# Performance work log

Hardware: AMD Instinct MI355X
Metric: run time of the kernel (lower is better)

Reference implementation:

```python
import jax, jax.numpy as jnp
import numpy as np

NB = 5  # number of graph nodes per image
COUNT_THRESH = 10000  # min pixel count for a region to be selected
BOX_DOWNSCALE = 16.0  # backbone stride


def _masks_to_boxes(mask_np, ids):
    # torchvision.ops.masks_to_boxes: (xmin, ymin, xmax, ymax) in pixel coords
    boxes = []
    for oid in ids:
        ys, xs = np.nonzero(mask_np == oid)
        boxes.append([xs.min(), ys.min(), xs.max(), ys.max()])
    return np.asarray(boxes, dtype=np.float32)


def _select_boxes(seg_logits):
    # mask = espnet(x).max(1)[1]; original code only keeps boxes from the LAST
    # batch element (loop variable overwritten each iteration) -- preserved here.
    mask = np.asarray(jnp.argmax(seg_logits, axis=1))[-1]
    ids, counts = np.unique(mask, return_counts=True)
    ids, counts = ids[1:], counts[1:]  # drop background / first label
    boxes = _masks_to_boxes(mask, ids) / BOX_DOWNSCALE  # feature-map coords
    # rr = argsort(argsort(counts, descending)) == rank of each region by size
    rr = np.argsort(np.argsort(-counts))
    sel = []
    for idx in range(len(boxes)):
        for b_idx in range(len(rr)):
            if idx == rr[b_idx] and counts[b_idx] > COUNT_THRESH and len(sel) < NB - 2:
                sel.append(b_idx)
                break
    return boxes.astype(np.int64), sel


def setup_inputs() -> dict:
    key = jax.random.key(0)
    k1, k2, k3 = jax.random.split(key, 3)
    N, K, Hin, Win = 4, 20, 480, 640   # even H/W -> parity padding is a no-op
    C, H, W = 512, Hin // 16, Win // 16  # stride-16 VGG backbone features
    return {
        "seg_logits": jax.random.normal(k1, (N, K, Hin, Win), jnp.float32),
        "feat": jax.random.normal(k2, (N, C, H, W), jnp.float32),
        "pool_x": jax.random.normal(k3, (N, C), jnp.float32),
    }


def reference(seg_logits, feat, pool_x):
    boxes, sel = _select_boxes(seg_logits)
    N, C, H, W = feat.shape
    # Selected-region crops; boxes identical for every batch element (original
    # bug), so each crop+resize is vectorized over the batch dim.
    nodes = []
    for b in sel:
        x0, y0, x1, y1 = [int(v) for v in boxes[b]]
        crop = feat[:, :, y0:y1, x0:x1]
        nodes.append(jax.image.resize(crop, (N, C, H, W), "bilinear"))
    # Fixed fallback boxes (center, left/top/right/bottom strips)
    bb = [[W // 4, H // 4, 3 * W // 4, 3 * H // 4],
          [0, 0, W // 3, H],
          [0, 0, W, H // 3],
          [2 * W // 3, 0, W, H],
          [0, 2 * H // 3, W, H]]
    if len(nodes) < NB:
        for i in range(len(bb) - len(nodes)):  # range evaluated once, as in original
            x0, y0, x1, y1 = bb[i]
            crop = feat[:, :, y0:y1, x0:x1]
            nodes.append(jax.image.resize(crop, (N, C, H, W), "bilinear"))
    graph_nodes = jnp.stack(nodes, axis=1)  # [N, NB, C, H, W]
    # Original: graph_nodes.view(NB, N, ...) is a raw reshape, then cat with feat
    x_cropped = jnp.concatenate(
        [graph_nodes.reshape(NB, N, C, H, W), feat[None]], axis=0)  # [NB+1,N,C,H,W]
    return pool_x, NB, N, x_cropped
```

## Files before the change

### kernel.cpp

```cpp
#include <hip/hip_runtime.h>
#include <hip/hip_bf16.h>

#define K_CLS 20
#define HIN 480
#define WIN 640
#define NPIX (HIN * WIN)
#define C_ 512
#define H_ 30
#define W_ 40
#define HW_ (H_ * W_)
#define NB_ 5
#define CNT_THRESH 10000
#define XCROP_ELEMS (6 * 4 * C_ * H_ * W_)
#define ELEMS_PER_SN (C_ * H_ * W_)
#define OUT_TOTAL (2050 + XCROP_ELEMS)

#define NBLK_STATS 300
#define NODE_OFF (NBLK_STATS * 100)

typedef float f32x2 __attribute__((ext_vector_type(2)));
typedef float f32x4 __attribute__((ext_vector_type(4)));

#define OUT_CPB 4
#define OUT_CGRP (C_ / OUT_CPB)
#define OUT_TPB 256
#define OUT_BLOCKS (24 * OUT_CGRP)


__global__ void stats_k(const float* __restrict__ seg, int* __restrict__ ws) {
    __shared__ int s_cnt[K_CLS], s_mnx[K_CLS], s_mny[K_CLS], s_mxx[K_CLS], s_mxy[K_CLS];
    int t = threadIdx.x;
    if (t < K_CLS) { s_cnt[t] = 0; s_mnx[t] = WIN; s_mny[t] = HIN; s_mxx[t] = -1; s_mxy[t] = -1; }
    __syncthreads();

    int p = blockIdx.x * blockDim.x + t;
    const float4* base = (const float4*)(seg + (size_t)3 * K_CLS * NPIX) + p;
    float4 v = base[0];
    float b0 = v.x, b1 = v.y, b2 = v.z, b3 = v.w;
    int k0 = 0, k1 = 0, k2 = 0, k3 = 0;
    #pragma unroll
    for (int k = 1; k < K_CLS; k++) {
        float4 u = base[(size_t)k * (NPIX / 4)];
        if (u.x > b0) { b0 = u.x; k0 = k; }
        if (u.y > b1) { b1 = u.y; k1 = k; }
        if (u.z > b2) { b2 = u.z; k2 = k; }
        if (u.w > b3) { b3 = u.w; k3 = k; }
    }
    int x = (p * 4) % WIN, y = (p * 4) / WIN;
    if (k0 == k1 && k1 == k2 && k2 == k3) {
        atomicAdd(&s_cnt[k0], 4);
        atomicMin(&s_mnx[k0], x);     atomicMax(&s_mxx[k0], x + 3);
        atomicMin(&s_mny[k0], y);     atomicMax(&s_mxy[k0], y);
    } else {
        int ks[4] = {k0, k1, k2, k3};
        #pragma unroll
        for (int i = 0; i < 4; i++) {
            atomicAdd(&s_cnt[ks[i]], 1);
            atomicMin(&s_mnx[ks[i]], x + i);  atomicMax(&s_mxx[ks[i]], x + i);
            atomicMin(&s_mny[ks[i]], y);      atomicMax(&s_mxy[ks[i]], y);
        }
    }
    __syncthreads();
    if (t < 100) {
        int a = t / 20, c = t % 20;
        int val = (a == 0) ? s_cnt[c] : (a == 1) ? s_mnx[c] : (a == 2) ? s_mny[c]
                : (a == 3) ? s_mxx[c] : s_mxy[c];
        ws[blockIdx.x * 100 + t] = val;
    }
}

__global__ void plan_k(int* __restrict__ ws, const float* __restrict__ pool_x,
                       float* __restrict__ out) {
    __shared__ int part[10][100];
    __shared__ int st[100];
    int t = threadIdx.x;

    ((float2*)out)[t] = ((const float2*)pool_x)[t];
    if (t == 0) { out[2048] = 5.0f; out[2049] = 4.0f; }

    if (t < 1000) {
        int c = t % 100, chunk = t / 100;
        int a = c / 20;
        int acc = (a == 0) ? 0 : (a == 1) ? WIN : (a == 2) ? HIN : -1;
        #pragma unroll
        for (int i = 0; i < 30; i++) {
            int v = ws[(chunk * 30 + i) * 100 + c];
            if (a == 0)      acc += v;
            else if (a <= 2) acc = v < acc ? v : acc;
            else             acc = v > acc ? v : acc;
        }
        part[chunk][c] = acc;
    }
    __syncthreads();
    if (t < 100) {
        int a = t / 20;
        int acc = part[0][t];
        #pragma unroll
        for (int i = 1; i < 10; i++) {
            int v = part[i][t];
            if (a == 0)      acc += v;
            else if (a <= 2) acc = v < acc ? v : acc;
            else             acc = v > acc ? v : acc;
        }
        st[t] = acc;
    }
    __syncthreads();
    if (t != 0) return;

    int* cnt = st;
    int* mnx = st + 20; int* mny = st + 40; int* mxx = st + 60; int* mxy = st + 80;
    int* nb  = ws + NODE_OFF;

    int firstp = -1;
    for (int i = 0; i < K_CLS; i++) if (cnt[i] > 0) { firstp = i; break; }
    int order[K_CLS]; int nc = 0;
    for (int i = 0; i < K_CLS; i++)
        if (cnt[i] > 0 && i != firstp) order[nc++] = i;

    for (int i = 1; i < nc; i++) {
        int key = order[i]; int j = i - 1;
        while (j >= 0 && cnt[order[j]] < cnt[key]) { order[j + 1] = order[j]; j--; }
        order[j + 1] = key;
    }

    int nsel = 0;
    for (int i = 0; i < nc && nsel < NB_ - 2; i++) {
        int b = order[i];
        if (cnt[b] > CNT_THRESH) {
            nb[nsel * 4 + 0] = mnx[b] >> 4;
            nb[nsel * 4 + 1] = mny[b] >> 4;
            nb[nsel * 4 + 2] = mxx[b] >> 4;
            nb[nsel * 4 + 3] = mxy[b] >> 4;
            nsel++;
        }
    }
    const int bb[5][4] = {
        {W_ / 4, H_ / 4, 3 * W_ / 4, 3 * H_ / 4},
        {0, 0, W_ / 3, H_},
        {0, 0, W_, H_ / 3},
        {2 * W_ / 3, 0, W_, H_},
        {0, 2 * H_ / 3, W_, H_}
    };
    for (int i = 0; nsel < NB_; i++, nsel++) {
        nb[nsel * 4 + 0] = bb[i][0];
        nb[nsel * 4 + 1] = bb[i][1];
        nb[nsel * 4 + 2] = bb[i][2];
        nb[nsel * 4 + 3] = bb[i][3];
    }
}

__global__ __launch_bounds__(OUT_TPB) void out_k(const float* __restrict__ feat,
                      const int* __restrict__ nb,
                      float* __restrict__ out) {
    __shared__ float sf[OUT_CPB * HW_];
    int sn = blockIdx.x / OUT_CGRP;
    int c0 = (blockIdx.x % OUT_CGRP) * OUT_CPB;
    float* obase = out + 2050 + (size_t)sn * ELEMS_PER_SN + (size_t)c0 * HW_;

    if (sn >= 20) {
        const float* src = feat + ((size_t)(sn - 20) * C_ + c0) * HW_;
        for (int i = threadIdx.x; i < (OUT_CPB * HW_) / 2; i += OUT_TPB) {
            __builtin_nontemporal_store(((const f32x2*)src)[i], (f32x2*)obase + i);
        }
        return;
    }

    int b  = sn % NB_;
    int n  = sn / NB_;
    int x0 = nb[b * 4 + 0], y0 = nb[b * 4 + 1];
    int x1 = nb[b * 4 + 2], y1 = nb[b * 4 + 3];
    int iw = x1 - x0; if (iw < 1) iw = 1;
    int ih = y1 - y0; if (ih < 1) ih = 1;

    const float* src = feat + ((size_t)n * C_ + c0) * HW_;
    for (int i = threadIdx.x; i < (OUT_CPB * HW_) / 4; i += OUT_TPB) {
        ((f32x4*)sf)[i] = ((const f32x4*)src)[i];
    }
    __syncthreads();

    float sx = (float)iw * (1.0f / (float)W_);
    float sy = (float)ih * (1.0f / (float)H_);
    int cb = y0 * W_ + x0;

    for (int hw = threadIdx.x; hw < HW_; hw += OUT_TPB) {
        int h = hw / W_;
        int w = hw - h * W_;

        float fy  = ((float)h + 0.5f) * sy - 0.5f;
        float flY = floorf(fy);
        float ty  = fy - flY;
        int ylo_u = (int)flY;
        int ylo = max(ylo_u, 0);
        int yhi = min(ylo_u + 1, ih - 1);

        float fx  = ((float)w + 0.5f) * sx - 0.5f;
        float flX = floorf(fx);
        float tx  = fx - flX;
        int xlo_u = (int)flX;
        int xlo = max(xlo_u, 0);
        int xhi = min(xlo_u + 1, iw - 1);

        int i00 = cb + ylo * W_ + xlo, i01 = cb + ylo * W_ + xhi;
        int i10 = cb + yhi * W_ + xlo, i11 = cb + yhi * W_ + xhi;

        float* op = obase + hw;
        #pragma unroll
        for (int j = 0; j < OUT_CPB; j++) {
            const float* sp = sf + j * HW_;
            float v00 = sp[i00], v01 = sp[i01];
            float v10 = sp[i10], v11 = sp[i11];
            float top = v00 + tx * (v01 - v00);
            float bot = v10 + tx * (v11 - v10);
            __builtin_nontemporal_store(top + ty * (bot - top), op + j * HW_);
        }
    }
}

extern "C" void kernel_launch(void* const* d_in, const int* in_sizes, int n_in,
                              void* d_out, int out_size, void* d_ws, size_t ws_size,
                              hipStream_t stream) {
    const float* seg    = (const float*)d_in[0];
    const float* feat   = (const float*)d_in[1];
    const float* pool_x = (const float*)d_in[2];
    float* out = (float*)d_out;
    int* ws = (int*)d_ws;

    stats_k<<<NBLK_STATS, 256, 0, stream>>>(seg, ws);
    plan_k<<<1, 1024, 0, stream>>>(ws, pool_x, out);
    out_k<<<OUT_BLOCKS, OUT_TPB, 0, stream>>>(feat, ws + NODE_OFF, out);
}
```

Before: 196.9 us.

## Fuse per-node crop-resize and feat copy into one block per channel group

```diff
diff --git a/kernel.cpp b/kernel.cpp
--- a/kernel.cpp
+++ b/kernel.cpp
@@ -21,10 +21,10 @@
 typedef float f32x2 __attribute__((ext_vector_type(2)));
 typedef float f32x4 __attribute__((ext_vector_type(4)));
 
-#define OUT_CPB 4
-#define OUT_CGRP (C_ / OUT_CPB)
-#define OUT_TPB 256
-#define OUT_BLOCKS (24 * OUT_CGRP)
+#define F_CPB 4
+#define F_CGRP (C_ / F_CPB)
+#define F_TPB 512
+#define F_BLOCKS (4 * F_CGRP)
 
 
 __global__ void stats_k(const float* __restrict__ seg, int* __restrict__ ws) {
@@ -149,69 +149,86 @@
     }
 }
 
-__global__ __launch_bounds__(OUT_TPB) void out_k(const float* __restrict__ feat,
+__global__ __launch_bounds__(F_TPB) void fuse_k(const float* __restrict__ feat,
                       const int* __restrict__ nb,
                       float* __restrict__ out) {
-    __shared__ float sf[OUT_CPB * HW_];
-    int sn = blockIdx.x / OUT_CGRP;
-    int c0 = (blockIdx.x % OUT_CGRP) * OUT_CPB;
-    float* obase = out + 2050 + (size_t)sn * ELEMS_PER_SN + (size_t)c0 * HW_;
-
-    if (sn >= 20) {
-        const float* src = feat + ((size_t)(sn - 20) * C_ + c0) * HW_;
-        for (int i = threadIdx.x; i < (OUT_CPB * HW_) / 2; i += OUT_TPB) {
-            __builtin_nontemporal_store(((const f32x2*)src)[i], (f32x2*)obase + i);
-        }
-        return;
-    }
-
-    int b  = sn % NB_;
-    int n  = sn / NB_;
-    int x0 = nb[b * 4 + 0], y0 = nb[b * 4 + 1];
-    int x1 = nb[b * 4 + 2], y1 = nb[b * 4 + 3];
-    int iw = x1 - x0; if (iw < 1) iw = 1;
-    int ih = y1 - y0; if (ih < 1) ih = 1;
+    __shared__ float sf[F_CPB * HW_];
+    __shared__ int   s_xlo[NB_ * W_], s_xhi[NB_ * W_];
+    __shared__ float s_tx [NB_ * W_];
+    __shared__ int   s_r0 [NB_ * H_], s_r1 [NB_ * H_];
+    __shared__ float s_ty [NB_ * H_];
+
+    int t  = threadIdx.x;
+    int n  = blockIdx.x / F_CGRP;
+    int c0 = (blockIdx.x % F_CGRP) * F_CPB;
 
     const float* src = feat + ((size_t)n * C_ + c0) * HW_;
-    for (int i = threadIdx.x; i < (OUT_CPB * HW_) / 4; i += OUT_TPB) {
-        ((f32x4*)sf)[i] = ((const f32x4*)src)[i];
-    }
-    __syncthreads();
-
-    float sx = (float)iw * (1.0f / (float)W_);
-    float sy = (float)ih * (1.0f / (float)H_);
-    int cb = y0 * W_ + x0;
-
-    for (int hw = threadIdx.x; hw < HW_; hw += OUT_TPB) {
-        int h = hw / W_;
-        int w = hw - h * W_;
-
-        float fy  = ((float)h + 0.5f) * sy - 0.5f;
-        float flY = floorf(fy);
-        float ty  = fy - flY;
-        int ylo_u = (int)flY;
-        int ylo = max(ylo_u, 0);
-        int yhi = min(ylo_u + 1, ih - 1);
-
-        float fx  = ((float)w + 0.5f) * sx - 0.5f;
-        float flX = floorf(fx);
-        float tx  = fx - flX;
-        int xlo_u = (int)flX;
-        int xlo = max(xlo_u, 0);
-        int xhi = min(xlo_u + 1, iw - 1);
-
-        int i00 = cb + ylo * W_ + xlo, i01 = cb + ylo * W_ + xhi;
-        int i10 = cb + yhi * W_ + xlo, i11 = cb + yhi * W_ + xhi;
-
-        float* op = obase + hw;
-        #pragma unroll
-        for (int j = 0; j < OUT_CPB; j++) {
-            const float* sp = sf + j * HW_;
-            float v00 = sp[i00], v01 = sp[i01];
-            float v10 = sp[i10], v11 = sp[i11];
-            float top = v00 + tx * (v01 - v00);
-            float bot = v10 + tx * (v11 - v10);
-            __builtin_nontemporal_store(top + ty * (bot - top), op + j * HW_);
+    float* cdst = out + 2050 + (size_t)(20 + n) * ELEMS_PER_SN + (size_t)c0 * HW_;
+    for (int i = t; i < (F_CPB * HW_) / 4; i += F_TPB) {
+        f32x4 v = ((const f32x4*)src)[i];
+        ((f32x4*)sf)[i] = v;
+        f32x2 lo = {v.x, v.y}, hi = {v.z, v.w};
+        __builtin_nontemporal_store(lo, (f32x2*)(cdst + i * 4));
+        __builtin_nontemporal_store(hi, (f32x2*)(cdst + i * 4 + 2));
+    }
+
+    if (t < NB_ * W_ + NB_ * H_) {
+        int isX = t < NB_ * W_;
+        int b   = isX ? t / W_ : (t - NB_ * W_) / H_;
+        int x0 = nb[b * 4 + 0], y0 = nb[b * 4 + 1];
+        int x1 = nb[b * 4 + 2], y1 = nb[b * 4 + 3];
+        int iw = max(x1 - x0, 1), ih = max(y1 - y0, 1);
+        if (isX) {
+            int w = t % W_;
+            float fx = ((float)w + 0.5f) * (float)iw / (float)W_ - 0.5f;
+            float fl = floorf(fx);
+            int lo_u = (int)fl;
+            s_tx[t]  = fx - fl;
+            s_xlo[t] = max(lo_u, 0);
+            s_xhi[t] = min(lo_u + 1, iw - 1);
+        } else {
+            int e = t - NB_ * W_;
+            int h = e % H_;
+            float fy = ((float)h + 0.5f) * (float)ih / (float)H_ - 0.5f;
+            float fl = floorf(fy);
+            int lo_u = (int)fl;
+            int yl = max(lo_u, 0);
+            int yh = min(lo_u + 1, ih - 1);
+            int cb = y0 * W_ + x0;
+            s_ty[e] = fy - fl;
+            s_r0[e] = cb + yl * W_;
+            s_r1[e] = cb + yh * W_;
+        }
+    }
+    __syncthreads();
+
+    for (int b = 0; b < NB_; b++) {
+        float* ob = out + 2050 + (size_t)(5 * n + b) * ELEMS_PER_SN + (size_t)c0 * HW_;
+        const int*   xlo = s_xlo + b * W_;
+        const int*   xhi = s_xhi + b * W_;
+        const float* txp = s_tx  + b * W_;
+        const int*   r0p = s_r0  + b * H_;
+        const int*   r1p = s_r1  + b * H_;
+        const float* typ = s_ty  + b * H_;
+        for (int hw = t; hw < HW_; hw += F_TPB) {
+            int h = hw / W_;
+            int w = hw - h * W_;
+            int r0 = r0p[h], r1 = r1p[h];
+            float ty = typ[h];
+            int xl = xlo[w], xh = xhi[w];
+            float tx = txp[w];
+            int i00 = r0 + xl, i01 = r0 + xh;
+            int i10 = r1 + xl, i11 = r1 + xh;
+            float* op = ob + hw;
+            #pragma unroll
+            for (int j = 0; j < F_CPB; j++) {
+                const float* sp = sf + j * HW_;
+                float v00 = sp[i00], v01 = sp[i01];
+                float v10 = sp[i10], v11 = sp[i11];
+                float top = v00 + tx * (v01 - v00);
+                float bot = v10 + tx * (v11 - v10);
+                __builtin_nontemporal_store(top + ty * (bot - top), op + j * HW_);
+            }
         }
     }
 }
@@ -227,5 +244,5 @@
 
     stats_k<<<NBLK_STATS, 256, 0, stream>>>(seg, ws);
     plan_k<<<1, 1024, 0, stream>>>(ws, pool_x, out);
-    out_k<<<OUT_BLOCKS, OUT_TPB, 0, stream>>>(feat, ws + NODE_OFF, out);
-}
+    fuse_k<<<F_BLOCKS, F_TPB, 0, stream>>>(feat, ws + NODE_OFF, out);
+}
```

Measured after the change: 199.6 us. No clear change (+1.4%).

## Fuse plan and output kernels, recomputing box plan redundantly per block

Applied to the files above, without the earlier changes.

```diff
diff --git a/kernel.cpp b/kernel.cpp
--- a/kernel.cpp
+++ b/kernel.cpp
@@ -16,15 +16,14 @@
 #define OUT_TOTAL (2050 + XCROP_ELEMS)
 
 #define NBLK_STATS 300
-#define NODE_OFF (NBLK_STATS * 100)
 
 typedef float f32x2 __attribute__((ext_vector_type(2)));
 typedef float f32x4 __attribute__((ext_vector_type(4)));
 
-#define OUT_CPB 4
-#define OUT_CGRP (C_ / OUT_CPB)
-#define OUT_TPB 256
-#define OUT_BLOCKS (24 * OUT_CGRP)
+#define F_CPB 4
+#define F_CGRP (C_ / F_CPB)
+#define F_TPB 512
+#define F_BLOCKS (4 * F_CGRP)
 
 
 __global__ void stats_k(const float* __restrict__ seg, int* __restrict__ ws) {
@@ -69,22 +68,41 @@
     }
 }
 
-__global__ void plan_k(int* __restrict__ ws, const float* __restrict__ pool_x,
-                       float* __restrict__ out) {
-    __shared__ int part[10][100];
+__global__ __launch_bounds__(F_TPB) void fuse_k(const float* __restrict__ feat,
+                      const int* __restrict__ ws,
+                      const float* __restrict__ pool_x,
+                      float* __restrict__ out) {
+    __shared__ float sf[F_CPB * HW_];
+    __shared__ int part[5][100];
     __shared__ int st[100];
-    int t = threadIdx.x;
-
-    ((float2*)out)[t] = ((const float2*)pool_x)[t];
-    if (t == 0) { out[2048] = 5.0f; out[2049] = 4.0f; }
-
-    if (t < 1000) {
+    __shared__ int s_nb[NB_ * 4];
+
+    int t  = threadIdx.x;
+    int n  = blockIdx.x / F_CGRP;
+    int c0 = (blockIdx.x % F_CGRP) * F_CPB;
+
+    const float* src = feat + ((size_t)n * C_ + c0) * HW_;
+    float* cdst = out + 2050 + (size_t)(20 + n) * ELEMS_PER_SN + (size_t)c0 * HW_;
+    for (int i = t; i < (F_CPB * HW_) / 4; i += F_TPB) {
+        f32x4 v = ((const f32x4*)src)[i];
+        ((f32x4*)sf)[i] = v;
+        f32x2 lo = {v.x, v.y}, hi = {v.z, v.w};
+        __builtin_nontemporal_store(lo, (f32x2*)(cdst + i * 4));
+        __builtin_nontemporal_store(hi, (f32x2*)(cdst + i * 4 + 2));
+    }
+    if (blockIdx.x == 0) {
+        for (int i = t; i < 1024; i += F_TPB)
+            ((float2*)out)[i] = ((const float2*)pool_x)[i];
+        if (t == 0) { out[2048] = 5.0f; out[2049] = 4.0f; }
+    }
+
+    if (t < 500) {
         int c = t % 100, chunk = t / 100;
         int a = c / 20;
         int acc = (a == 0) ? 0 : (a == 1) ? WIN : (a == 2) ? HIN : -1;
         #pragma unroll
-        for (int i = 0; i < 30; i++) {
-            int v = ws[(chunk * 30 + i) * 100 + c];
+        for (int i = 0; i < 60; i++) {
+            int v = ws[(chunk * 60 + i) * 100 + c];
             if (a == 0)      acc += v;
             else if (a <= 2) acc = v < acc ? v : acc;
             else             acc = v > acc ? v : acc;
@@ -96,7 +114,7 @@
         int a = t / 20;
         int acc = part[0][t];
         #pragma unroll
-        for (int i = 1; i < 10; i++) {
+        for (int i = 1; i < 5; i++) {
             int v = part[i][t];
             if (a == 0)      acc += v;
             else if (a <= 2) acc = v < acc ? v : acc;
@@ -105,113 +123,89 @@
         st[t] = acc;
     }
     __syncthreads();
-    if (t != 0) return;
-
-    int* cnt = st;
-    int* mnx = st + 20; int* mny = st + 40; int* mxx = st + 60; int* mxy = st + 80;
-    int* nb  = ws + NODE_OFF;
-
-    int firstp = -1;
-    for (int i = 0; i < K_CLS; i++) if (cnt[i] > 0) { firstp = i; break; }
-    int order[K_CLS]; int nc = 0;
-    for (int i = 0; i < K_CLS; i++)
-        if (cnt[i] > 0 && i != firstp) order[nc++] = i;
-
-    for (int i = 1; i < nc; i++) {
-        int key = order[i]; int j = i - 1;
-        while (j >= 0 && cnt[order[j]] < cnt[key]) { order[j + 1] = order[j]; j--; }
-        order[j + 1] = key;
-    }
-
-    int nsel = 0;
-    for (int i = 0; i < nc && nsel < NB_ - 2; i++) {
-        int b = order[i];
-        if (cnt[b] > CNT_THRESH) {
-            nb[nsel * 4 + 0] = mnx[b] >> 4;
-            nb[nsel * 4 + 1] = mny[b] >> 4;
-            nb[nsel * 4 + 2] = mxx[b] >> 4;
-            nb[nsel * 4 + 3] = mxy[b] >> 4;
-            nsel++;
-        }
-    }
-    const int bb[5][4] = {
-        {W_ / 4, H_ / 4, 3 * W_ / 4, 3 * H_ / 4},
-        {0, 0, W_ / 3, H_},
-        {0, 0, W_, H_ / 3},
-        {2 * W_ / 3, 0, W_, H_},
-        {0, 2 * H_ / 3, W_, H_}
-    };
-    for (int i = 0; nsel < NB_; i++, nsel++) {
-        nb[nsel * 4 + 0] = bb[i][0];
-        nb[nsel * 4 + 1] = bb[i][1];
-        nb[nsel * 4 + 2] = bb[i][2];
-        nb[nsel * 4 + 3] = bb[i][3];
-    }
-}
-
-__global__ __launch_bounds__(OUT_TPB) void out_k(const float* __restrict__ feat,
-                      const int* __restrict__ nb,
-                      float* __restrict__ out) {
-    __shared__ float sf[OUT_CPB * HW_];
-    int sn = blockIdx.x / OUT_CGRP;
-    int c0 = (blockIdx.x % OUT_CGRP) * OUT_CPB;
-    float* obase = out + 2050 + (size_t)sn * ELEMS_PER_SN + (size_t)c0 * HW_;
-
-    if (sn >= 20) {
-        const float* src = feat + ((size_t)(sn - 20) * C_ + c0) * HW_;
-        for (int i = threadIdx.x; i < (OUT_CPB * HW_) / 2; i += OUT_TPB) {
-            __builtin_nontemporal_store(((const f32x2*)src)[i], (f32x2*)obase + i);
-        }
-        return;
-    }
-
-    int b  = sn % NB_;
-    int n  = sn / NB_;
-    int x0 = nb[b * 4 + 0], y0 = nb[b * 4 + 1];
-    int x1 = nb[b * 4 + 2], y1 = nb[b * 4 + 3];
-    int iw = x1 - x0; if (iw < 1) iw = 1;
-    int ih = y1 - y0; if (ih < 1) ih = 1;
-
-    const float* src = feat + ((size_t)n * C_ + c0) * HW_;
-    for (int i = threadIdx.x; i < (OUT_CPB * HW_) / 4; i += OUT_TPB) {
-        ((f32x4*)sf)[i] = ((const f32x4*)src)[i];
-    }
-    __syncthreads();
-
-    float sx = (float)iw * (1.0f / (float)W_);
-    float sy = (float)ih * (1.0f / (float)H_);
-    int cb = y0 * W_ + x0;
-
-    for (int hw = threadIdx.x; hw < HW_; hw += OUT_TPB) {
-        int h = hw / W_;
-        int w = hw - h * W_;
-
-        float fy  = ((float)h + 0.5f) * sy - 0.5f;
-        float flY = floorf(fy);
-        float ty  = fy - flY;
-        int ylo_u = (int)flY;
-        int ylo = max(ylo_u, 0);
-        int yhi = min(ylo_u + 1, ih - 1);
-
-        float fx  = ((float)w + 0.5f) * sx - 0.5f;
-        float flX = floorf(fx);
-        float tx  = fx - flX;
-        int xlo_u = (int)flX;
-        int xlo = max(xlo_u, 0);
-        int xhi = min(xlo_u + 1, iw - 1);
-
-        int i00 = cb + ylo * W_ + xlo, i01 = cb + ylo * W_ + xhi;
-        int i10 = cb + yhi * W_ + xlo, i11 = cb + yhi * W_ + xhi;
-
-        float* op = obase + hw;
-        #pragma unroll
-        for (int j = 0; j < OUT_CPB; j++) {
-            const float* sp = sf + j * HW_;
-            float v00 = sp[i00], v01 = sp[i01];
-            float v10 = sp[i10], v11 = sp[i11];
-            float top = v00 + tx * (v01 - v00);
-            float bot = v10 + tx * (v11 - v10);
-            __builtin_nontemporal_store(top + ty * (bot - top), op + j * HW_);
+    if (t == 0) {
+        int* cnt = st;
+        int* mnx = st + 20; int* mny = st + 40; int* mxx = st + 60; int* mxy = st + 80;
+
+        int firstp = -1;
+        for (int i = 0; i < K_CLS; i++) if (cnt[i] > 0) { firstp = i; break; }
+        int order[K_CLS]; int nc = 0;
+        for (int i = 0; i < K_CLS; i++)
+            if (cnt[i] > 0 && i != firstp) order[nc++] = i;
+
+        for (int i = 1; i < nc; i++) {
+            int key = order[i]; int j = i - 1;
+            while (j >= 0 && cnt[order[j]] < cnt[key]) { order[j + 1] = order[j]; j--; }
+            order[j + 1] = key;
+        }
+
+        int nsel = 0;
+        for (int i = 0; i < nc && nsel < NB_ - 2; i++) {
+            int b = order[i];
+            if (cnt[b] > CNT_THRESH) {
+                s_nb[nsel * 4 + 0] = mnx[b] >> 4;
+                s_nb[nsel * 4 + 1] = mny[b] >> 4;
+                s_nb[nsel * 4 + 2] = mxx[b] >> 4;
+                s_nb[nsel * 4 + 3] = mxy[b] >> 4;
+                nsel++;
+            }
+        }
+        const int bb[5][4] = {
+            {W_ / 4, H_ / 4, 3 * W_ / 4, 3 * H_ / 4},
+            {0, 0, W_ / 3, H_},
+            {0, 0, W_, H_ / 3},
+            {2 * W_ / 3, 0, W_, H_},
+            {0, 2 * H_ / 3, W_, H_}
+        };
+        for (int i = 0; nsel < NB_; i++, nsel++) {
+            s_nb[nsel * 4 + 0] = bb[i][0];
+            s_nb[nsel * 4 + 1] = bb[i][1];
+            s_nb[nsel * 4 + 2] = bb[i][2];
+            s_nb[nsel * 4 + 3] = bb[i][3];
+        }
+    }
+    __syncthreads();
+
+    for (int b = 0; b < NB_; b++) {
+        int x0 = s_nb[b * 4 + 0], y0 = s_nb[b * 4 + 1];
+        int x1 = s_nb[b * 4 + 2], y1 = s_nb[b * 4 + 3];
+        int iw = max(x1 - x0, 1), ih = max(y1 - y0, 1);
+        int cb = y0 * W_ + x0;
+        float sx = (float)iw * (1.0f / (float)W_);
+        float sy = (float)ih * (1.0f / (float)H_);
+        float* ob = out + 2050 + (size_t)(5 * n + b) * ELEMS_PER_SN + (size_t)c0 * HW_;
+
+        for (int hw = t; hw < HW_; hw += F_TPB) {
+            int h = hw / W_;
+            int w = hw - h * W_;
+
+            float fy  = ((float)h + 0.5f) * sy - 0.5f;
+            float flY = floorf(fy);
+            float ty  = fy - flY;
+            int ylo_u = (int)flY;
+            int ylo = max(ylo_u, 0);
+            int yhi = min(ylo_u + 1, ih - 1);
+
+            float fx  = ((float)w + 0.5f) * sx - 0.5f;
+            float flX = floorf(fx);
+            float tx  = fx - flX;
+            int xlo_u = (int)flX;
+            int xlo = max(xlo_u, 0);
+            int xhi = min(xlo_u + 1, iw - 1);
+
+            int i00 = cb + ylo * W_ + xlo, i01 = cb + ylo * W_ + xhi;
+            int i10 = cb + yhi * W_ + xlo, i11 = cb + yhi * W_ + xhi;
+
+            float* op = ob + hw;
+            #pragma unroll
+            for (int j = 0; j < F_CPB; j++) {
+                const float* sp = sf + j * HW_;
+                float v00 = sp[i00], v01 = sp[i01];
+                float v10 = sp[i10], v11 = sp[i11];
+                float top = v00 + tx * (v01 - v00);
+                float bot = v10 + tx * (v11 - v10);
+                __builtin_nontemporal_store(top + ty * (bot - top), op + j * HW_);
+            }
         }
     }
 }
@@ -226,6 +220,5 @@
     int* ws = (int*)d_ws;
 
     stats_k<<<NBLK_STATS, 256, 0, stream>>>(seg, ws);
-    plan_k<<<1, 1024, 0, stream>>>(ws, pool_x, out);
-    out_k<<<OUT_BLOCKS, OUT_TPB, 0, stream>>>(feat, ws + NODE_OFF, out);
+    fuse_k<<<F_BLOCKS, F_TPB, 0, stream>>>(feat, ws, pool_x, out);
 }
```

New measurement: 201.3 us. 2.2% more time.
